# Performance work log

Measured on AMD Instinct MI355X. Metric: run time of the kernel, lower is better.

The kernel has to match this reference:

```python
import jax, jax.numpy as jnp
import numpy as np

PATCH_H, PATCH_W = 14, 14
N = PATCH_H * PATCH_W

def _build_adjacency(H, W):
    A = np.zeros((H * W, H * W), dtype=np.float32)
    for i in range(H):
        for j in range(W):
            idx = i * W + j
            for ni, nj in [(i - 1, j), (i + 1, j), (i, j - 1), (i, j + 1)]:
                if 0 <= ni < H and 0 <= nj < W:
                    A[idx, ni * W + nj] = 1.0
    return jnp.asarray(A)

A_ADJ = _build_adjacency(PATCH_H, PATCH_W)          # [N, N]
I_EYE = jnp.eye(N, dtype=jnp.float32)               # [N, N]

def setup_inputs() -> dict:
    key = jax.random.key(0)
    k1, k2 = jax.random.split(key)
    B, C = 256, 768
    S = jax.random.normal(k1, (B, C, PATCH_H, PATCH_W), dtype=jnp.float32)
    attn = jax.random.uniform(k2, (B, 1, PATCH_H, PATCH_W), dtype=jnp.float32)
    lmbd = jnp.array([2.0], dtype=jnp.float32)
    beta = jnp.array([0.1], dtype=jnp.float32)
    return {"S": S, "attn": attn, "lmbd": lmbd, "beta": beta}

def reference(S, attn, lmbd, beta):
    B, C, H, W = S.shape
    lm = lmbd[0]
    bt = beta[0]
    attn5 = attn * 5.0                                      # [B,1,H,W]
    # L2-normalize over channel dim (torch F.normalize, eps=1e-12)
    S_flat = S.reshape(B, C, N)                             # [B,C,N]
    norm = jnp.sqrt(jnp.sum(S_flat * S_flat, axis=1, keepdims=True))
    S_flat = S_flat / jnp.maximum(norm, 1e-12)
    # patch-patch similarity Gram matrix
    E = jnp.einsum('bcn,bcm->bnm', S_flat, S_flat)          # [B,N,N]
    E = (E + 1.0) * 0.5
    # graph Laplacian weighted by attention-modulated similarity
    deg = jnp.sum(A_ADJ, axis=-1)                           # [N]
    DmA = jnp.diag(deg) - A_ADJ                             # [N,N]
    L = DmA[None, :, :] * (lm * E - 1.0) + 1e-6 * I_EYE[None, :, :]
    # Newton-Schulz iterations for pseudo-inverse
    X = jnp.swapaxes(L, -1, -2) * 0.01
    twoI = 2.0 * I_EYE[None, :, :]
    for _ in range(4):
        X = X @ (twoI - L @ X)
    # diffuse attention through pseudo-inverse
    Fd = jnp.einsum('bnm,bm->bn', X, attn5.reshape(B, N))   # [B,N]
    F_diff = bt * (Fd - jnp.tanh(Fd / (bt + 1e-8)))         # tanh-shrinkage
    F_map = F_diff.reshape(B, 1, H, W)
    S_new = S * (1.0 + F_map)
    return (S_new, F_map)
```

## Files before the change

kernel.cpp:

```cpp
#include <hip/hip_runtime.h>
#include <cstdint>

#define PN 196
#define PC 768
#define KC 16

template<int NCH>
__global__ __launch_bounds__(256) void adb_reduce(
    const float* __restrict__ S, float* __restrict__ partials)
{
    constexpr int CPB = PC / NCH;
    const int b   = blockIdx.y;
    const int ch  = blockIdx.x;
    const int tid = threadIdx.x;

    __shared__ __align__(16) float rows[KC * PN + 16];

    const float* Sb = S + (size_t)b * PC * PN + (size_t)ch * CPB * PN;

    const bool lane = tid < PN;
    const int n = lane ? tid : 0;

    float acc_s = 0.f, acc_r = 0.f, acc_d = 0.f;

    for (int c0 = 0; c0 < CPB; c0 += KC) {
        __syncthreads();
        const float4* src = (const float4*)(Sb + c0 * PN);
        float4* dst = (float4*)rows;
        #pragma unroll
        for (int k = 0; k < 4; k++) {
            int idx = tid + k * 256;
            if (idx < KC * PN / 4) dst[idx] = src[idx];
        }
        __syncthreads();
        if (lane) {
            const float* r0 = rows + n;
            #pragma unroll
            for (int cc = 0; cc < KC; cc++) {
                const float* r = r0 + cc * PN;
                float s = r[0];
                acc_s += s * s;
                acc_r += s * r[1];
                acc_d += s * r[14];
            }
        }
    }

    if (lane) {
        float* P = partials + ((size_t)b * NCH + ch) * 3 * PN;
        P[0 * PN + n] = acc_s;
        P[1 * PN + n] = acc_r;
        P[2 * PN + n] = acc_d;
    }
}

template<int NCH>
__global__ __launch_bounds__(64) void adb_solve(
    const float* __restrict__ partials, const float* __restrict__ attn,
    const float* __restrict__ lmbd, const float* __restrict__ beta,
    float* __restrict__ Fmap, float* __restrict__ Gmap)
{
    const int b  = blockIdx.x;
    const int L  = threadIdx.x;
    const int i2 = L / 7, j2 = L % 7;
    const bool act = (L < 49) && (i2 < 7);

    const int n00 = act ? ((2 * i2) * 14 + 2 * j2) : 0;
    const int nn0 = n00, nn1 = n00 + 1, nn2 = n00 + 14, nn3 = n00 + 15;

    float as0 = 0.f, as1 = 0.f, as2 = 0.f, as3 = 0.f;
    float ar0 = 0.f, ar1 = 0.f, ar2 = 0.f, ar3 = 0.f;
    float ad0 = 0.f, ad1 = 0.f, ad2 = 0.f, ad3 = 0.f;
    if (act) {
        const float* P = partials + (size_t)b * NCH * 3 * PN;
        #pragma unroll
        for (int ch = 0; ch < NCH; ch++) {
            const float* Pc = P + ch * 3 * PN;
            as0 += Pc[nn0]; as1 += Pc[nn1]; as2 += Pc[nn2]; as3 += Pc[nn3];
            ar0 += Pc[PN + nn0]; ar1 += Pc[PN + nn1];
            ar2 += Pc[PN + nn2]; ar3 += Pc[PN + nn3];
            ad0 += Pc[2 * PN + nn0]; ad1 += Pc[2 * PN + nn1];
            ad2 += Pc[2 * PN + nn2]; ad3 += Pc[2 * PN + nn3];
        }
    }

    const float lm = lmbd[0];
    const float bt = beta[0];

    float rn0 = 1.0f / fmaxf(sqrtf(as0), 1e-12f);
    float rn1 = 1.0f / fmaxf(sqrtf(as1), 1e-12f);
    float rn2 = 1.0f / fmaxf(sqrtf(as2), 1e-12f);
    float rn3 = 1.0f / fmaxf(sqrtf(as3), 1e-12f);

    const int sl_l = (j2 > 0) ? L - 1 : L;
    const int sl_r = (j2 < 6) ? L + 1 : L;
    const int sl_u = (i2 > 0) ? L - 7 : L;
    const int sl_d = (i2 < 6) ? L + 7 : L;

    float rnL0 = __shfl(rn1, sl_l, 64);
    float rnL2 = __shfl(rn3, sl_l, 64);
    float rnR1 = __shfl(rn0, sl_r, 64);
    float rnR3 = __shfl(rn2, sl_r, 64);
    float rnU0 = __shfl(rn2, sl_u, 64);
    float rnU1 = __shfl(rn3, sl_u, 64);
    float rnD2 = __shfl(rn0, sl_d, 64);
    float rnD3 = __shfl(rn1, sl_d, 64);
    float srL0 = __shfl(ar1, sl_l, 64);
    float srL2 = __shfl(ar3, sl_l, 64);
    float sdU0 = __shfl(ad2, sl_u, 64);
    float sdU1 = __shfl(ad3, sl_u, 64);

    const bool hl0 = (j2 > 0), hl2 = (j2 > 0);
    const bool hr1 = (j2 < 6), hr3 = (j2 < 6);
    const bool hu0 = (i2 > 0), hu1 = (i2 > 0);
    const bool hd2 = (i2 < 6), hd3 = (i2 < 6);

    const float deg0 = (hl0 ? 1.f : 0.f) + 1.f + (hu0 ? 1.f : 0.f) + 1.f;
    const float deg1 = 1.f + (hr1 ? 1.f : 0.f) + (hu1 ? 1.f : 0.f) + 1.f;
    const float deg2 = (hl2 ? 1.f : 0.f) + 1.f + 1.f + (hd2 ? 1.f : 0.f);
    const float deg3 = 1.f + (hr3 ? 1.f : 0.f) + 1.f + (hd3 ? 1.f : 0.f);

    auto cdiag = [&](float as, float rn, float deg) {
        float Enn = (as * rn * rn + 1.f) * 0.5f;
        return deg * (lm * Enn - 1.f) + 1e-6f;
    };
    auto coff = [&](float dot, float rna, float rnb) {
        return 1.f - lm * ((dot * rna * rnb + 1.f) * 0.5f);
    };

    const float Lc0 = cdiag(as0, rn0, deg0);
    const float Lc1 = cdiag(as1, rn1, deg1);
    const float Lc2 = cdiag(as2, rn2, deg2);
    const float Lc3 = cdiag(as3, rn3, deg3);

    const float Ll0 = hl0 ? coff(srL0, rn0, rnL0) : 0.f;
    const float Ll1 =       coff(ar0,  rn1, rn0);
    const float Ll2 = hl2 ? coff(srL2, rn2, rnL2) : 0.f;
    const float Ll3 =       coff(ar2,  rn3, rn2);

    const float Lr0 =       coff(ar0,  rn0, rn1);
    const float Lr1 = hr1 ? coff(ar1,  rn1, rnR1) : 0.f;
    const float Lr2 =       coff(ar2,  rn2, rn3);
    const float Lr3 = hr3 ? coff(ar3,  rn3, rnR3) : 0.f;

    const float Lu0 = hu0 ? coff(sdU0, rn0, rnU0) : 0.f;
    const float Lu1 = hu1 ? coff(sdU1, rn1, rnU1) : 0.f;
    const float Lu2 =       coff(ad0,  rn2, rn0);
    const float Lu3 =       coff(ad1,  rn3, rn1);

    const float Ld0 =       coff(ad0,  rn0, rn2);
    const float Ld1 =       coff(ad1,  rn1, rn3);
    const float Ld2 = hd2 ? coff(ad2,  rn2, rnD2) : 0.f;
    const float Ld3 = hd3 ? coff(ad3,  rn3, rnD3) : 0.f;

    auto mv = [&](float& y0, float& y1, float& y2, float& y3,
                  float x0, float x1, float x2, float x3) {
        float xl0 = __shfl(x1, sl_l, 64);
        float xl2 = __shfl(x3, sl_l, 64);
        float xr1 = __shfl(x0, sl_r, 64);
        float xr3 = __shfl(x2, sl_r, 64);
        float xu0 = __shfl(x2, sl_u, 64);
        float xu1 = __shfl(x3, sl_u, 64);
        float xd2 = __shfl(x0, sl_d, 64);
        float xd3 = __shfl(x1, sl_d, 64);
        y0 = Lc0 * x0 + Ll0 * xl0 + Lr0 * x1  + Lu0 * xu0 + Ld0 * x2;
        y1 = Lc1 * x1 + Ll1 * x0  + Lr1 * xr1 + Lu1 * xu1 + Ld1 * x3;
        y2 = Lc2 * x2 + Ll2 * xl2 + Lr2 * x3  + Lu2 * x0  + Ld2 * xd2;
        y3 = Lc3 * x3 + Ll3 * x2  + Lr3 * xr3 + Lu3 * x1  + Ld3 * xd3;
    };

    float a0 = 0.f, a1 = 0.f, a2 = 0.f, a3 = 0.f;
    if (act) {
        const float* Ab = attn + (size_t)b * PN;
        a0 = Ab[nn0] * 5.0f; a1 = Ab[nn1] * 5.0f;
        a2 = Ab[nn2] * 5.0f; a3 = Ab[nn3] * 5.0f;
    }

    float v0, v1, v2, v3;
    mv(v0, v1, v2, v3, a0, a1, a2, a3);
    v0 *= 0.01f; v1 *= 0.01f; v2 *= 0.01f; v3 *= 0.01f;

    #pragma unroll
    for (int stage = 0; stage < 4; stage++) {
        float w0 = v0, w1 = v1, w2 = v2, w3 = v3;
        const int k = 1 << stage;
        for (int it = 0; it < k; it++) {
            float t0, t1, t2, t3, s0, s1, s2, s3;
            mv(t0, t1, t2, t3, w0, w1, w2, w3);
            mv(s0, s1, s2, s3, t0, t1, t2, t3);
            w0 -= 0.01f * s0; w1 -= 0.01f * s1;
            w2 -= 0.01f * s2; w3 -= 0.01f * s3;
        }
        v0 += w0; v1 += w1; v2 += w2; v3 += w3;
    }

    if (act) {
        auto shrink = [&](float Fd) {
            return bt * (Fd - tanhf(Fd / (bt + 1e-8f)));
        };
        float f0 = shrink(v0), f1 = shrink(v1), f2 = shrink(v2), f3 = shrink(v3);
        float* Fb = Fmap + (size_t)b * PN;
        float* Gb = Gmap + (size_t)b * PN;
        Fb[nn0] = f0; Fb[nn1] = f1; Fb[nn2] = f2; Fb[nn3] = f3;
        Gb[nn0] = 1.0f + f0; Gb[nn1] = 1.0f + f1;
        Gb[nn2] = 1.0f + f2; Gb[nn3] = 1.0f + f3;
    }
}

__global__ __launch_bounds__(256) void adb_scale(
    const float* __restrict__ S, const float* __restrict__ Gmap,
    float* __restrict__ out)
{
    const int b   = blockIdx.y;
    const int tid = threadIdx.x;

    __shared__ float Gs[PN + 3];
    const float* Gb = Gmap + (size_t)b * PN;
    if (tid < PN / 4) ((float4*)Gs)[tid] = ((const float4*)Gb)[tid];
    if (tid >= 64 && tid < 67) Gs[PN + (tid - 64)] = Gb[tid - 64];
    __syncthreads();

    const int off = blockIdx.x * 1024 + tid * 4;
    const int n0  = off % PN;
    const size_t base = (size_t)b * PC * PN + off;
    float4 sv = *(const float4*)(S + base);
    float4 o;
    o.x = sv.x * Gs[n0];
    o.y = sv.y * Gs[n0 + 1];
    o.z = sv.z * Gs[n0 + 2];
    o.w = sv.w * Gs[n0 + 3];
    *(float4*)(out + base) = o;
}

extern "C" void kernel_launch(void* const* d_in, const int* in_sizes, int n_in,
                              void* d_out, int out_size, void* d_ws, size_t ws_size,
                              hipStream_t stream) {
    const float* S    = (const float*)d_in[0];
    const float* attn = (const float*)d_in[1];
    const float* lmbd = (const float*)d_in[2];
    const float* beta = (const float*)d_in[3];

    const int B = in_sizes[1] / PN;

    float* Snew = (float*)d_out;
    float* Fmap = (float*)d_out + (size_t)B * PC * PN;
    float* ws   = (float*)d_ws;

    const size_t need8 = ((size_t)B * 8 * 3 * PN + (size_t)B * PN) * sizeof(float);
    const size_t need2 = ((size_t)B * 2 * 3 * PN + (size_t)B * PN) * sizeof(float);
    const size_t need1 = ((size_t)B * 1 * 3 * PN + (size_t)B * PN) * sizeof(float);

    if (ws_size >= need8) {
        float* partials = ws;
        float* Gmap = ws + (size_t)B * 8 * 3 * PN;
        adb_reduce<8><<<dim3(8, B), 256, 0, stream>>>(S, partials);
        adb_solve<8><<<B, 64, 0, stream>>>(partials, attn, lmbd, beta, Fmap, Gmap);
        adb_scale<<<dim3((PC * PN) / 1024, B), 256, 0, stream>>>(S, Gmap, Snew);
    } else if (ws_size >= need2) {
        float* partials = ws;
        float* Gmap = ws + (size_t)B * 2 * 3 * PN;
        adb_reduce<2><<<dim3(2, B), 256, 0, stream>>>(S, partials);
        adb_solve<2><<<B, 64, 0, stream>>>(partials, attn, lmbd, beta, Fmap, Gmap);
        adb_scale<<<dim3((PC * PN) / 1024, B), 256, 0, stream>>>(S, Gmap, Snew);
    } else {
        float* partials = ws;
        float* Gmap = ws + (size_t)B * 1 * 3 * PN;
        (void)need1;
        adb_reduce<1><<<dim3(1, B), 256, 0, stream>>>(S, partials);
        adb_solve<1><<<B, 64, 0, stream>>>(partials, attn, lmbd, beta, Fmap, Gmap);
        adb_scale<<<dim3((PC * PN) / 1024, B), 256, 0, stream>>>(S, Gmap, Snew);
    }
}
```

Measured before the change: 299.7 us.

## Fuse reduce, solve and scale into one per-batch 1024-thread kernel

Replaces the three-kernel pipeline (partial channel reductions, per-batch Newton-Schulz solve, elementwise scale) with a single kernel that runs one 1024-thread block per batch. Four 256-thread groups each reduce a quarter of the channels into shared memory. The partials are combined in shared memory, one wave runs the stencil solve, and then the whole block scales S using nontemporal stores. This removes the workspace round-trips, two launches and the separate Gmap pass, and it may let the second read of S hit in cache. In exchange the grid is only B blocks with synchronous load/compute phases, and most of the block sits idle during the serial solve, which can reduce memory-level parallelism.

```diff
diff --git a/kernel.cpp b/kernel.cpp
--- a/kernel.cpp
+++ b/kernel.cpp
@@ -4,37 +4,65 @@
 #define PN 196
 #define PC 768
 #define KC 16
-
-template<int NCH>
-__global__ __launch_bounds__(256) void adb_reduce(
-    const float* __restrict__ S, float* __restrict__ partials)
+#define NG 4
+#define CPG (PC / NG)
+
+typedef float f32x4_t __attribute__((ext_vector_type(4)));
+
+__global__ __launch_bounds__(1024) void adb_fused(
+    const float* __restrict__ S, const float* __restrict__ attn,
+    const float* __restrict__ lmbd, const float* __restrict__ beta,
+    float* __restrict__ out, float* __restrict__ Fmap)
 {
-    constexpr int CPB = PC / NCH;
-    const int b   = blockIdx.y;
-    const int ch  = blockIdx.x;
+    const int b   = blockIdx.x;
     const int tid = threadIdx.x;
-
-    __shared__ __align__(16) float rows[KC * PN + 16];
-
-    const float* Sb = S + (size_t)b * PC * PN + (size_t)ch * CPB * PN;
-
-    const bool lane = tid < PN;
-    const int n = lane ? tid : 0;
+    const int g   = tid >> 8;
+    const int t   = tid & 255;
+
+    __shared__ __align__(16) float rows[NG][KC * PN + 16];
+    __shared__ float pS[NG][PN];
+    __shared__ float pR[NG][PN];
+    __shared__ float pD[NG][PN];
+    __shared__ __align__(16) float Gs[PN];
+
+    const size_t bbase = (size_t)b * PC * PN;
+
+    const bool sw  = (tid < 64);
+    const int  i2  = tid / 7, j2 = tid % 7;
+    const bool act = sw && (tid < 49);
+    const int  n00 = act ? ((2 * i2) * 14 + 2 * j2) : 0;
+    float a0 = 0.f, a1 = 0.f, a2 = 0.f, a3 = 0.f, lm = 0.f, bt = 0.f;
+    if (sw) {
+        lm = lmbd[0];
+        bt = beta[0];
+        if (act) {
+            const float* Ab = attn + (size_t)b * PN;
+            a0 = Ab[n00]      * 5.0f;
+            a1 = Ab[n00 + 1]  * 5.0f;
+            a2 = Ab[n00 + 14] * 5.0f;
+            a3 = Ab[n00 + 15] * 5.0f;
+        }
+    }
+
+    const bool lane = t < PN;
+    const int  n    = lane ? t : 0;
+
+    const float* Sg = S + bbase + (size_t)g * CPG * PN;
 
     float acc_s = 0.f, acc_r = 0.f, acc_d = 0.f;
 
-    for (int c0 = 0; c0 < CPB; c0 += KC) {
+    for (int c0 = 0; c0 < CPG; c0 += KC) {
         __syncthreads();
-        const float4* src = (const float4*)(Sb + c0 * PN);
-        float4* dst = (float4*)rows;
+        const float4* src = (const float4*)(Sg + c0 * PN);
+        float4* dst = (float4*)rows[g];
         #pragma unroll
         for (int k = 0; k < 4; k++) {
-            int idx = tid + k * 256;
+            int idx = t + k * 256;
             if (idx < KC * PN / 4) dst[idx] = src[idx];
         }
         __syncthreads();
         if (lane) {
-            const float* r0 = rows + n;
+            const float* r0 = rows[g] + n;
             #pragma unroll
             for (int cc = 0; cc < KC; cc++) {
                 const float* r = r0 + cc * PN;
@@ -46,190 +74,160 @@
         }
     }
 
-    if (lane) {
-        float* P = partials + ((size_t)b * NCH + ch) * 3 * PN;
-        P[0 * PN + n] = acc_s;
-        P[1 * PN + n] = acc_r;
-        P[2 * PN + n] = acc_d;
-    }
-}
-
-template<int NCH>
-__global__ __launch_bounds__(64) void adb_solve(
-    const float* __restrict__ partials, const float* __restrict__ attn,
-    const float* __restrict__ lmbd, const float* __restrict__ beta,
-    float* __restrict__ Fmap, float* __restrict__ Gmap)
-{
-    const int b  = blockIdx.x;
-    const int L  = threadIdx.x;
-    const int i2 = L / 7, j2 = L % 7;
-    const bool act = (L < 49) && (i2 < 7);
-
-    const int n00 = act ? ((2 * i2) * 14 + 2 * j2) : 0;
-    const int nn0 = n00, nn1 = n00 + 1, nn2 = n00 + 14, nn3 = n00 + 15;
-
-    float as0 = 0.f, as1 = 0.f, as2 = 0.f, as3 = 0.f;
-    float ar0 = 0.f, ar1 = 0.f, ar2 = 0.f, ar3 = 0.f;
-    float ad0 = 0.f, ad1 = 0.f, ad2 = 0.f, ad3 = 0.f;
-    if (act) {
-        const float* P = partials + (size_t)b * NCH * 3 * PN;
+    if (lane) { pS[g][n] = acc_s; pR[g][n] = acc_r; pD[g][n] = acc_d; }
+    __syncthreads();
+
+    if (tid < 3 * PN) {
+        const int axis = tid / PN;
+        const int nn   = tid - axis * PN;
+        float* base = (axis == 0) ? &pS[0][0]
+                    : (axis == 1) ? &pR[0][0] : &pD[0][0];
+        base[nn] = base[nn] + base[PN + nn] + base[2 * PN + nn]
+                 + base[3 * PN + nn];
+    }
+    __syncthreads();
+
+    if (sw) {
+        const int L = tid;
+
+        const float as0 = pS[0][n00],      as1 = pS[0][n00 + 1];
+        const float as2 = pS[0][n00 + 14], as3 = pS[0][n00 + 15];
+        const float ar0 = pR[0][n00],      ar1 = pR[0][n00 + 1];
+        const float ar2 = pR[0][n00 + 14], ar3 = pR[0][n00 + 15];
+        const float ad0 = pD[0][n00],      ad1 = pD[0][n00 + 1];
+        const float ad2 = pD[0][n00 + 14], ad3 = pD[0][n00 + 15];
+
+        float rn0 = 1.0f / fmaxf(sqrtf(as0), 1e-12f);
+        float rn1 = 1.0f / fmaxf(sqrtf(as1), 1e-12f);
+        float rn2 = 1.0f / fmaxf(sqrtf(as2), 1e-12f);
+        float rn3 = 1.0f / fmaxf(sqrtf(as3), 1e-12f);
+
+        const int sl_l = (j2 > 0) ? L - 1 : L;
+        const int sl_r = (j2 < 6) ? L + 1 : L;
+        const int sl_u = (i2 > 0) ? L - 7 : L;
+        const int sl_d = (i2 < 6) ? L + 7 : L;
+
+        float rnL0 = __shfl(rn1, sl_l, 64);
+        float rnL2 = __shfl(rn3, sl_l, 64);
+        float rnR1 = __shfl(rn0, sl_r, 64);
+        float rnR3 = __shfl(rn2, sl_r, 64);
+        float rnU0 = __shfl(rn2, sl_u, 64);
+        float rnU1 = __shfl(rn3, sl_u, 64);
+        float rnD2 = __shfl(rn0, sl_d, 64);
+        float rnD3 = __shfl(rn1, sl_d, 64);
+        float srL0 = __shfl(ar1, sl_l, 64);
+        float srL2 = __shfl(ar3, sl_l, 64);
+        float sdU0 = __shfl(ad2, sl_u, 64);
+        float sdU1 = __shfl(ad3, sl_u, 64);
+
+        const bool hl = (j2 > 0), hr = (j2 < 6), hu = (i2 > 0), hd = (i2 < 6);
+
+        const float deg0 = (hl ? 1.f : 0.f) + 1.f + (hu ? 1.f : 0.f) + 1.f;
+        const float deg1 = 1.f + (hr ? 1.f : 0.f) + (hu ? 1.f : 0.f) + 1.f;
+        const float deg2 = (hl ? 1.f : 0.f) + 1.f + 1.f + (hd ? 1.f : 0.f);
+        const float deg3 = 1.f + (hr ? 1.f : 0.f) + 1.f + (hd ? 1.f : 0.f);
+
+        auto cdiag = [&](float as, float rn, float deg) {
+            float Enn = (as * rn * rn + 1.f) * 0.5f;
+            return deg * (lm * Enn - 1.f) + 1e-6f;
+        };
+        auto coff = [&](float dot, float rna, float rnb) {
+            return 1.f - lm * ((dot * rna * rnb + 1.f) * 0.5f);
+        };
+
+        const float Lc0 = cdiag(as0, rn0, deg0);
+        const float Lc1 = cdiag(as1, rn1, deg1);
+        const float Lc2 = cdiag(as2, rn2, deg2);
+        const float Lc3 = cdiag(as3, rn3, deg3);
+
+        const float Ll0 = hl ? coff(srL0, rn0, rnL0) : 0.f;
+        const float Ll1 =      coff(ar0,  rn1, rn0);
+        const float Ll2 = hl ? coff(srL2, rn2, rnL2) : 0.f;
+        const float Ll3 =      coff(ar2,  rn3, rn2);
+
+        const float Lr0 =      coff(ar0,  rn0, rn1);
+        const float Lr1 = hr ? coff(ar1,  rn1, rnR1) : 0.f;
+        const float Lr2 =      coff(ar2,  rn2, rn3);
+        const float Lr3 = hr ? coff(ar3,  rn3, rnR3) : 0.f;
+
+        const float Lu0 = hu ? coff(sdU0, rn0, rnU0) : 0.f;
+        const float Lu1 = hu ? coff(sdU1, rn1, rnU1) : 0.f;
+        const float Lu2 =      coff(ad0,  rn2, rn0);
+        const float Lu3 =      coff(ad1,  rn3, rn1);
+
+        const float Ld0 =      coff(ad0,  rn0, rn2);
+        const float Ld1 =      coff(ad1,  rn1, rn3);
+        const float Ld2 = hd ? coff(ad2,  rn2, rnD2) : 0.f;
+        const float Ld3 = hd ? coff(ad3,  rn3, rnD3) : 0.f;
+
+        auto mv = [&](float& y0, float& y1, float& y2, float& y3,
+                      float x0, float x1, float x2, float x3) {
+            float xl0 = __shfl(x1, sl_l, 64);
+            float xl2 = __shfl(x3, sl_l, 64);
+            float xr1 = __shfl(x0, sl_r, 64);
+            float xr3 = __shfl(x2, sl_r, 64);
+            float xu0 = __shfl(x2, sl_u, 64);
+            float xu1 = __shfl(x3, sl_u, 64);
+            float xd2 = __shfl(x0, sl_d, 64);
+            float xd3 = __shfl(x1, sl_d, 64);
+            y0 = Lc0 * x0 + Ll0 * xl0 + Lr0 * x1  + Lu0 * xu0 + Ld0 * x2;
+            y1 = Lc1 * x1 + Ll1 * x0  + Lr1 * xr1 + Lu1 * xu1 + Ld1 * x3;
+            y2 = Lc2 * x2 + Ll2 * xl2 + Lr2 * x3  + Lu2 * x0  + Ld2 * xd2;
+            y3 = Lc3 * x3 + Ll3 * x2  + Lr3 * xr3 + Lu3 * x1  + Ld3 * xd3;
+        };
+
+        float v0, v1, v2, v3;
+        mv(v0, v1, v2, v3, a0, a1, a2, a3);
+        v0 *= 0.01f; v1 *= 0.01f; v2 *= 0.01f; v3 *= 0.01f;
+
         #pragma unroll
-        for (int ch = 0; ch < NCH; ch++) {
-            const float* Pc = P + ch * 3 * PN;
-            as0 += Pc[nn0]; as1 += Pc[nn1]; as2 += Pc[nn2]; as3 += Pc[nn3];
-            ar0 += Pc[PN + nn0]; ar1 += Pc[PN + nn1];
-            ar2 += Pc[PN + nn2]; ar3 += Pc[PN + nn3];
-            ad0 += Pc[2 * PN + nn0]; ad1 += Pc[2 * PN + nn1];
-            ad2 += Pc[2 * PN + nn2]; ad3 += Pc[2 * PN + nn3];
-        }
-    }
-
-    const float lm = lmbd[0];
-    const float bt = beta[0];
-
-    float rn0 = 1.0f / fmaxf(sqrtf(as0), 1e-12f);
-    float rn1 = 1.0f / fmaxf(sqrtf(as1), 1e-12f);
-    float rn2 = 1.0f / fmaxf(sqrtf(as2), 1e-12f);
-    float rn3 = 1.0f / fmaxf(sqrtf(as3), 1e-12f);
-
-    const int sl_l = (j2 > 0) ? L - 1 : L;
-    const int sl_r = (j2 < 6) ? L + 1 : L;
-    const int sl_u = (i2 > 0) ? L - 7 : L;
-    const int sl_d = (i2 < 6) ? L + 7 : L;
-
-    float rnL0 = __shfl(rn1, sl_l, 64);
-    float rnL2 = __shfl(rn3, sl_l, 64);
-    float rnR1 = __shfl(rn0, sl_r, 64);
-    float rnR3 = __shfl(rn2, sl_r, 64);
-    float rnU0 = __shfl(rn2, sl_u, 64);
-    float rnU1 = __shfl(rn3, sl_u, 64);
-    float rnD2 = __shfl(rn0, sl_d, 64);
-    float rnD3 = __shfl(rn1, sl_d, 64);
-    float srL0 = __shfl(ar1, sl_l, 64);
-    float srL2 = __shfl(ar3, sl_l, 64);
-    float sdU0 = __shfl(ad2, sl_u, 64);
-    float sdU1 = __shfl(ad3, sl_u, 64);
-
-    const bool hl0 = (j2 > 0), hl2 = (j2 > 0);
-    const bool hr1 = (j2 < 6), hr3 = (j2 < 6);
-    const bool hu0 = (i2 > 0), hu1 = (i2 > 0);
-    const bool hd2 = (i2 < 6), hd3 = (i2 < 6);
-
-    const float deg0 = (hl0 ? 1.f : 0.f) + 1.f + (hu0 ? 1.f : 0.f) + 1.f;
-    const float deg1 = 1.f + (hr1 ? 1.f : 0.f) + (hu1 ? 1.f : 0.f) + 1.f;
-    const float deg2 = (hl2 ? 1.f : 0.f) + 1.f + 1.f + (hd2 ? 1.f : 0.f);
-    const float deg3 = 1.f + (hr3 ? 1.f : 0.f) + 1.f + (hd3 ? 1.f : 0.f);
-
-    auto cdiag = [&](float as, float rn, float deg) {
-        float Enn = (as * rn * rn + 1.f) * 0.5f;
-        return deg * (lm * Enn - 1.f) + 1e-6f;
-    };
-    auto coff = [&](float dot, float rna, float rnb) {
-        return 1.f - lm * ((dot * rna * rnb + 1.f) * 0.5f);
-    };
-
-    const float Lc0 = cdiag(as0, rn0, deg0);
-    const float Lc1 = cdiag(as1, rn1, deg1);
-    const float Lc2 = cdiag(as2, rn2, deg2);
-    const float Lc3 = cdiag(as3, rn3, deg3);
-
-    const float Ll0 = hl0 ? coff(srL0, rn0, rnL0) : 0.f;
-    const float Ll1 =       coff(ar0,  rn1, rn0);
-    const float Ll2 = hl2 ? coff(srL2, rn2, rnL2) : 0.f;
-    const float Ll3 =       coff(ar2,  rn3, rn2);
-
-    const float Lr0 =       coff(ar0,  rn0, rn1);
-    const float Lr1 = hr1 ? coff(ar1,  rn1, rnR1) : 0.f;
-    const float Lr2 =       coff(ar2,  rn2, rn3);
-    const float Lr3 = hr3 ? coff(ar3,  rn3, rnR3) : 0.f;
-
-    const float Lu0 = hu0 ? coff(sdU0, rn0, rnU0) : 0.f;
-    const float Lu1 = hu1 ? coff(sdU1, rn1, rnU1) : 0.f;
-    const float Lu2 =       coff(ad0,  rn2, rn0);
-    const float Lu3 =       coff(ad1,  rn3, rn1);
-
-    const float Ld0 =       coff(ad0,  rn0, rn2);
-    const float Ld1 =       coff(ad1,  rn1, rn3);
-    const float Ld2 = hd2 ? coff(ad2,  rn2, rnD2) : 0.f;
-    const float Ld3 = hd3 ? coff(ad3,  rn3, rnD3) : 0.f;
-
-    auto mv = [&](float& y0, float& y1, float& y2, float& y3,
-                  float x0, float x1, float x2, float x3) {
-        float xl0 = __shfl(x1, sl_l, 64);
-        float xl2 = __shfl(x3, sl_l, 64);
-        float xr1 = __shfl(x0, sl_r, 64);
-        float xr3 = __shfl(x2, sl_r, 64);
-        float xu0 = __shfl(x2, sl_u, 64);
-        float xu1 = __shfl(x3, sl_u, 64);
-        float xd2 = __shfl(x0, sl_d, 64);
-        float xd3 = __shfl(x1, sl_d, 64);
-        y0 = Lc0 * x0 + Ll0 * xl0 + Lr0 * x1  + Lu0 * xu0 + Ld0 * x2;
-        y1 = Lc1 * x1 + Ll1 * x0  + Lr1 * xr1 + Lu1 * xu1 + Ld1 * x3;
-        y2 = Lc2 * x2 + Ll2 * xl2 + Lr2 * x3  + Lu2 * x0  + Ld2 * xd2;
-        y3 = Lc3 * x3 + Ll3 * x2  + Lr3 * xr3 + Lu3 * x1  + Ld3 * xd3;
-    };
-
-    float a0 = 0.f, a1 = 0.f, a2 = 0.f, a3 = 0.f;
-    if (act) {
-        const float* Ab = attn + (size_t)b * PN;
-        a0 = Ab[nn0] * 5.0f; a1 = Ab[nn1] * 5.0f;
-        a2 = Ab[nn2] * 5.0f; a3 = Ab[nn3] * 5.0f;
-    }
-
-    float v0, v1, v2, v3;
-    mv(v0, v1, v2, v3, a0, a1, a2, a3);
-    v0 *= 0.01f; v1 *= 0.01f; v2 *= 0.01f; v3 *= 0.01f;
-
-    #pragma unroll
-    for (int stage = 0; stage < 4; stage++) {
-        float w0 = v0, w1 = v1, w2 = v2, w3 = v3;
-        const int k = 1 << stage;
-        for (int it = 0; it < k; it++) {
-            float t0, t1, t2, t3, s0, s1, s2, s3;
-            mv(t0, t1, t2, t3, w0, w1, w2, w3);
-            mv(s0, s1, s2, s3, t0, t1, t2, t3);
-            w0 -= 0.01f * s0; w1 -= 0.01f * s1;
-            w2 -= 0.01f * s2; w3 -= 0.01f * s3;
-        }
-        v0 += w0; v1 += w1; v2 += w2; v3 += w3;
-    }
-
-    if (act) {
-        auto shrink = [&](float Fd) {
-            return bt * (Fd - tanhf(Fd / (bt + 1e-8f)));
-        };
-        float f0 = shrink(v0), f1 = shrink(v1), f2 = shrink(v2), f3 = shrink(v3);
-        float* Fb = Fmap + (size_t)b * PN;
-        float* Gb = Gmap + (size_t)b * PN;
-        Fb[nn0] = f0; Fb[nn1] = f1; Fb[nn2] = f2; Fb[nn3] = f3;
-        Gb[nn0] = 1.0f + f0; Gb[nn1] = 1.0f + f1;
-        Gb[nn2] = 1.0f + f2; Gb[nn3] = 1.0f + f3;
-    }
-}
-
-__global__ __launch_bounds__(256) void adb_scale(
-    const float* __restrict__ S, const float* __restrict__ Gmap,
-    float* __restrict__ out)
-{
-    const int b   = blockIdx.y;
-    const int tid = threadIdx.x;
-
-    __shared__ float Gs[PN + 3];
-    const float* Gb = Gmap + (size_t)b * PN;
-    if (tid < PN / 4) ((float4*)Gs)[tid] = ((const float4*)Gb)[tid];
-    if (tid >= 64 && tid < 67) Gs[PN + (tid - 64)] = Gb[tid - 64];
+        for (int stage = 0; stage < 4; stage++) {
+            float w0 = v0, w1 = v1, w2 = v2, w3 = v3;
+            const int k = 1 << stage;
+            for (int it = 0; it < k; it++) {
+                float t0, t1, t2, t3, s0, s1, s2, s3;
+                mv(t0, t1, t2, t3, w0, w1, w2, w3);
+                mv(s0, s1, s2, s3, t0, t1, t2, t3);
+                w0 -= 0.01f * s0; w1 -= 0.01f * s1;
+                w2 -= 0.01f * s2; w3 -= 0.01f * s3;
+            }
+            v0 += w0; v1 += w1; v2 += w2; v3 += w3;
+        }
+
+        if (act) {
+            auto shrink = [&](float Fd) {
+                return bt * (Fd - tanhf(Fd / (bt + 1e-8f)));
+            };
+            float f0 = shrink(v0), f1 = shrink(v1);
+            float f2 = shrink(v2), f3 = shrink(v3);
+            float* Fb = Fmap + (size_t)b * PN;
+            Fb[n00]      = f0; Fb[n00 + 1]  = f1;
+            Fb[n00 + 14] = f2; Fb[n00 + 15] = f3;
+            Gs[n00]      = 1.0f + f0; Gs[n00 + 1]  = 1.0f + f1;
+            Gs[n00 + 14] = 1.0f + f2; Gs[n00 + 15] = 1.0f + f3;
+        }
+    }
     __syncthreads();
 
-    const int off = blockIdx.x * 1024 + tid * 4;
-    const int n0  = off % PN;
-    const size_t base = (size_t)b * PC * PN + off;
-    float4 sv = *(const float4*)(S + base);
-    float4 o;
-    o.x = sv.x * Gs[n0];
-    o.y = sv.y * Gs[n0 + 1];
-    o.z = sv.z * Gs[n0 + 2];
-    o.w = sv.w * Gs[n0 + 3];
-    *(float4*)(out + base) = o;
+    const f32x4_t* __restrict__ Gq = (const f32x4_t*)Gs;
+    const float*   __restrict__ Sb = S + bbase;
+    float*         __restrict__ Ob = out + bbase;
+
+    #pragma unroll 4
+    for (int k = 0; k < 36; k++) {
+        const int idx = k * 1024 + tid;
+        const int q   = idx % 49;
+        f32x4_t sv = *(const f32x4_t*)(Sb + (size_t)idx * 4);
+        f32x4_t o  = sv * Gq[q];
+        __builtin_nontemporal_store(o, (f32x4_t*)(Ob + (size_t)idx * 4));
+    }
+    if (tid < 768) {
+        const int idx = 36 * 1024 + tid;
+        const int q   = idx % 49;
+        f32x4_t sv = *(const f32x4_t*)(Sb + (size_t)idx * 4);
+        f32x4_t o  = sv * Gq[q];
+        __builtin_nontemporal_store(o, (f32x4_t*)(Ob + (size_t)idx * 4));
+    }
 }
 
 extern "C" void kernel_launch(void* const* d_in, const int* in_sizes, int n_in,
@@ -244,30 +242,7 @@
 
     float* Snew = (float*)d_out;
     float* Fmap = (float*)d_out + (size_t)B * PC * PN;
-    float* ws   = (float*)d_ws;
-
-    const size_t need8 = ((size_t)B * 8 * 3 * PN + (size_t)B * PN) * sizeof(float);
-    const size_t need2 = ((size_t)B * 2 * 3 * PN + (size_t)B * PN) * sizeof(float);
-    const size_t need1 = ((size_t)B * 1 * 3 * PN + (size_t)B * PN) * sizeof(float);
-
-    if (ws_size >= need8) {
-        float* partials = ws;
-        float* Gmap = ws + (size_t)B * 8 * 3 * PN;
-        adb_reduce<8><<<dim3(8, B), 256, 0, stream>>>(S, partials);
-        adb_solve<8><<<B, 64, 0, stream>>>(partials, attn, lmbd, beta, Fmap, Gmap);
-        adb_scale<<<dim3((PC * PN) / 1024, B), 256, 0, stream>>>(S, Gmap, Snew);
-    } else if (ws_size >= need2) {
-        float* partials = ws;
-        float* Gmap = ws + (size_t)B * 2 * 3 * PN;
-        adb_reduce<2><<<dim3(2, B), 256, 0, stream>>>(S, partials);
-        adb_solve<2><<<B, 64, 0, stream>>>(partials, attn, lmbd, beta, Fmap, Gmap);
-        adb_scale<<<dim3((PC * PN) / 1024, B), 256, 0, stream>>>(S, Gmap, Snew);
-    } else {
-        float* partials = ws;
-        float* Gmap = ws + (size_t)B * 1 * 3 * PN;
-        (void)need1;
-        adb_reduce<1><<<dim3(1, B), 256, 0, stream>>>(S, partials);
-        adb_solve<1><<<B, 64, 0, stream>>>(partials, attn, lmbd, beta, Fmap, Gmap);
-        adb_scale<<<dim3((PC * PN) / 1024, B), 256, 0, stream>>>(S, Gmap, Snew);
-    }
+    (void)d_ws; (void)ws_size;
+
+    adb_fused<<<B, 1024, 0, stream>>>(S, attn, lmbd, beta, Snew, Fmap);
 }
```

Result: faster. 292.8 us (-2.3%).
